# Kernel tuning notes

Measured on AMD Instinct MI355X. Metric: run time of the kernel, lower is better.

Reference implementation:

```python
import jax, jax.numpy as jnp
import numpy as np

N, D, E, P = 50000, 64, 800000, 2  # nodes, emb_dim, edges, pos dim


def setup_inputs() -> dict:
    key = jax.random.key(0)
    ks = jax.random.split(key, 20)
    s = 0.02  # gpt2-style init scale
    inp = {
        "h": jax.random.normal(ks[0], (N, D), jnp.float32),
        "pos": jax.random.uniform(ks[1], (N, P), jnp.float32),
        "h_init": jax.random.normal(ks[2], (N, D), jnp.float32),
        # edge MLP phi_e: [h_i, h_j, d2] -> D -> D
        "W_msg1": s * jax.random.normal(ks[3], (2 * D + 1, D), jnp.float32),
        "b_msg1": jnp.zeros((D,), jnp.float32),
        "W_msg2": s * jax.random.normal(ks[4], (D, D), jnp.float32),
        "b_msg2": jnp.zeros((D,), jnp.float32),
        # coord MLP phi_x: D -> D -> 1
        "W_pos1": s * jax.random.normal(ks[5], (D, D), jnp.float32),
        "b_pos1": jnp.zeros((D,), jnp.float32),
        "W_pos2": s * jax.random.normal(ks[6], (D, 1), jnp.float32),
        "b_pos2": jnp.zeros((1,), jnp.float32),
        # node MLP phi_h: [h, agg] -> D -> D
        "W_h1": s * jax.random.normal(ks[7], (2 * D, D), jnp.float32),
        "b_h1": jnp.zeros((D,), jnp.float32),
        "W_h2": s * jax.random.normal(ks[8], (D, D), jnp.float32),
        "b_h2": jnp.zeros((D,), jnp.float32),
        "edge_index": jax.random.randint(ks[9], (2, E), 0, N, jnp.int64),
    }
    return inp


def _egnn(h, pos, edge_index, W_msg1, b_msg1, W_msg2, b_msg2,
          W_pos1, b_pos1, W_pos2, b_pos2, W_h1, b_h1, W_h2, b_h2):
    src, dst = edge_index[0], edge_index[1]  # message j(src) -> i(dst)
    rel = pos[dst] - pos[src]                                  # [E,P]
    d2 = jnp.sum(rel * rel, axis=-1, keepdims=True)            # [E,1]
    m_in = jnp.concatenate([h[dst], h[src], d2], axis=-1)      # [E,2D+1]
    m = jax.nn.silu(jax.nn.silu(m_in @ W_msg1 + b_msg1) @ W_msg2 + b_msg2)  # [E,D]
    # coordinate update: mean_j rel_ij * phi_x(m_ij)
    w = jax.nn.silu(m @ W_pos1 + b_pos1) @ W_pos2 + b_pos2     # [E,1]
    n = h.shape[0]
    deg = jax.ops.segment_sum(jnp.ones((m.shape[0],), h.dtype), dst, num_segments=n)
    pos_update = jax.ops.segment_sum(rel * w, dst, num_segments=n) / jnp.maximum(deg, 1.0)[:, None]
    # feature update: phi_h([h, sum_j m_ij])
    agg = jax.ops.segment_sum(m, dst, num_segments=n)          # [N,D]
    h_update = jax.nn.silu(jnp.concatenate([h, agg], axis=-1) @ W_h1 + b_h1) @ W_h2 + b_h2
    return h_update, pos_update


def reference(h, pos, h_init, W_msg1, b_msg1, W_msg2, b_msg2,
              W_pos1, b_pos1, W_pos2, b_pos2, W_h1, b_h1, W_h2, b_h2,
              edge_index):
    # SpatialNCA.forward: add_init=True, skip_connections=True
    h = h + h_init
    h_update, pos_update = _egnn(h, pos, edge_index, W_msg1, b_msg1, W_msg2, b_msg2,
                                 W_pos1, b_pos1, W_pos2, b_pos2, W_h1, b_h1, W_h2, b_h2)
    return h + h_update, pos + pos_update
```

## Files before the change

### kernel.cpp

```cpp
#include <hip/hip_runtime.h>
#include <hip/hip_bf16.h>

#define N_NODES 50000
#define DIM 64
#define N_EDGES 800000
#define NTILES (N_EDGES / 16)
#define NODE_TILES (N_NODES / 16)

typedef short short8 __attribute__((ext_vector_type(8)));
typedef float f32x4 __attribute__((ext_vector_type(4)));

__device__ __forceinline__ float silu_f(float x) {
    return x * __builtin_amdgcn_rcpf(1.0f + __expf(-x));
}
__device__ __forceinline__ short f2bf(float f) {
    unsigned u = __builtin_bit_cast(unsigned, f);
    u += 0x7FFFu + ((u >> 16) & 1u);
    return (short)(u >> 16);
}
__device__ __forceinline__ void atom_pk_bf16(void* addr, unsigned data) {
    asm volatile("global_atomic_pk_add_bf16 %0, %1, off"
                 :: "v"((unsigned long long)(uintptr_t)addr), "v"(data) : "memory");
}

__global__ void k_init(const float* __restrict__ h, const float* __restrict__ h_init,
                       short* __restrict__ hpb, int* __restrict__ aggz,
                       float* __restrict__ posw3,
                       const void* __restrict__ eidx, int* __restrict__ eidx32) {
    __shared__ int sIs64;
    if (threadIdx.x == 0) {
        const int* e = (const int*)eidx;
        int f = 1;
        for (int k = 0; k < 64; ++k) if (e[2 * k + 1] != 0) { f = 0; break; }
        sIs64 = f;
    }
    __syncthreads();
    const int is64 = sIs64;

    int i = blockIdx.x * blockDim.x + threadIdx.x;
    int stride = gridDim.x * blockDim.x;
    for (int idx = i; idx < N_NODES * DIM; idx += stride)
        hpb[idx] = f2bf(h[idx] + h_init[idx]);
    for (int idx = i; idx < N_NODES * 32; idx += stride) aggz[idx] = 0;
    for (int idx = i; idx < N_NODES * 4; idx += stride) posw3[idx] = 0.0f;

    const long long* e64 = (const long long*)eidx;
    const int* e32 = (const int*)eidx;
    for (int idx = i; idx < 2 * N_EDGES; idx += stride)
        eidx32[idx] = is64 ? (int)e64[idx] : e32[idx];
}

__global__ __launch_bounds__(512, 6)
void k_edge(const short* __restrict__ hpb, const float* __restrict__ pos,
            const int* __restrict__ ei,
            const float* __restrict__ Wm1, const float* __restrict__ bm1,
            const float* __restrict__ Wm2, const float* __restrict__ bm2,
            const float* __restrict__ Wp1, const float* __restrict__ bp1,
            const float* __restrict__ Wp2, const float* __restrict__ bp2,
            short* __restrict__ aggb, float* __restrict__ posw3)
{
    __shared__ short sW1[8192];
    __shared__ short sW2[4096];
    __shared__ short sWp[4096];
    __shared__ short sT[8][1024];

    for (int i = threadIdx.x; i < 8192; i += 512) {
        int j = i & 7, lane = (i >> 3) & 63, nt = (i >> 9) & 3, kk = i >> 11;
        int k = kk * 32 + ((lane >> 4) << 3) + j;
        int n = (nt << 4) + (lane & 15);
        sW1[i] = f2bf(Wm1[k * 64 + n]);
    }
    for (int i = threadIdx.x; i < 4096; i += 512) {
        int j = i & 7, lane = (i >> 3) & 63, nt = (i >> 9) & 3, kk = i >> 11;
        int k = kk * 32 + ((lane >> 4) << 3) + j;
        int n = (nt << 4) + (lane & 15);
        sW2[i] = f2bf(Wm2[k * 64 + n]);
        sWp[i] = f2bf(Wp1[k * 64 + n]);
    }
    __syncthreads();

    const int lane = threadIdx.x & 63;
    const int wv   = threadIdx.x >> 6;
    const int g    = lane >> 4;
    const int c    = lane & 15;
    short* tile = &sT[wv][0];

    float bi1[4], bi2[4], bip[4], wp2r[4], w128f[4];
    #pragma unroll
    for (int nt = 0; nt < 4; ++nt) {
        bi1[nt]   = bm1[nt * 16 + c];
        bi2[nt]   = bm2[nt * 16 + c];
        bip[nt]   = bp1[nt * 16 + c];
        wp2r[nt]  = Wp2[nt * 16 + c];
        w128f[nt] = Wm1[128 * 64 + nt * 16 + c];
    }
    const float bp2v = bp2[0];

    const int gw = blockIdx.x * 8 + wv;
    const int nw = gridDim.x * 8;

    int s0 = 0, d0 = 0, s1 = 0, d1 = 0;
    float2 pd0 = {0.f, 0.f}, ps0 = {0.f, 0.f};
    short8 f0, f1, f2, f3;
    if (gw < NTILES) {
        int e = gw * 16 + c;
        s0 = ei[e]; d0 = ei[N_EDGES + e];
        pd0 = *(const float2*)(pos + (size_t)d0 * 2);
        ps0 = *(const float2*)(pos + (size_t)s0 * 2);
        f0 = *(const short8*)&hpb[(size_t)d0 * 64 + g * 8];
        f1 = *(const short8*)&hpb[(size_t)d0 * 64 + 32 + g * 8];
        f2 = *(const short8*)&hpb[(size_t)s0 * 64 + g * 8];
        f3 = *(const short8*)&hpb[(size_t)s0 * 64 + 32 + g * 8];
    }
    if (gw + nw < NTILES) {
        int e = (gw + nw) * 16 + c;
        s1 = ei[e]; d1 = ei[N_EDGES + e];
    }

    for (int t = gw; t < NTILES; t += nw) {
        const bool hasN  = (t + nw) < NTILES;
        const bool hasNN = (t + 2 * nw) < NTILES;

        float relx = pd0.x - ps0.x, rely = pd0.y - ps0.y;
        float dist2 = relx * relx + rely * rely;

        f32x4 acc[4];
        #pragma unroll
        for (int nt = 0; nt < 4; ++nt) acc[nt] = f32x4{0.f, 0.f, 0.f, 0.f};
        #pragma unroll
        for (int nt = 0; nt < 4; ++nt) {
            short8 b0 = *(const short8*)&sW1[((0 * 4 + nt) << 9) + (lane << 3)];
            short8 b1 = *(const short8*)&sW1[((1 * 4 + nt) << 9) + (lane << 3)];
            short8 b2 = *(const short8*)&sW1[((2 * 4 + nt) << 9) + (lane << 3)];
            short8 b3 = *(const short8*)&sW1[((3 * 4 + nt) << 9) + (lane << 3)];
            acc[nt] = __builtin_amdgcn_mfma_f32_16x16x32_bf16(f0, b0, acc[nt], 0, 0, 0);
            acc[nt] = __builtin_amdgcn_mfma_f32_16x16x32_bf16(f1, b1, acc[nt], 0, 0, 0);
            acc[nt] = __builtin_amdgcn_mfma_f32_16x16x32_bf16(f2, b2, acc[nt], 0, 0, 0);
            acc[nt] = __builtin_amdgcn_mfma_f32_16x16x32_bf16(f3, b3, acc[nt], 0, 0, 0);
        }

        short8 g0, g1, g2, g3;
        float2 pd1, ps1;
        if (hasN) {
            pd1 = *(const float2*)(pos + (size_t)d1 * 2);
            ps1 = *(const float2*)(pos + (size_t)s1 * 2);
            g0 = *(const short8*)&hpb[(size_t)d1 * 64 + g * 8];
            g1 = *(const short8*)&hpb[(size_t)d1 * 64 + 32 + g * 8];
            g2 = *(const short8*)&hpb[(size_t)s1 * 64 + g * 8];
            g3 = *(const short8*)&hpb[(size_t)s1 * 64 + 32 + g * 8];
        }
        int s2 = 0, d2i = 0;
        if (hasNN) {
            int e = (t + 2 * nw) * 16 + c;
            s2 = ei[e]; d2i = ei[N_EDGES + e];
        }

        float d2q[4];
        #pragma unroll
        for (int r = 0; r < 4; ++r) d2q[r] = __shfl(dist2, g * 4 + r, 64);
        #pragma unroll
        for (int nt = 0; nt < 4; ++nt) {
            #pragma unroll
            for (int r = 0; r < 4; ++r) {
                float v = silu_f(fmaf(d2q[r], w128f[nt], acc[nt][r] + bi1[nt]));
                int row = g * 4 + r;
                int idx = ((row << 6) + (nt << 4) + c) ^ ((row & 7) << 3);
                tile[idx] = f2bf(v);
            }
        }
        asm volatile("s_waitcnt lgkmcnt(0)" ::: "memory");
        __builtin_amdgcn_sched_barrier(0);

        short8 a20, a21;
        {
            int row = c;
            int b0 = ((row << 6) + (g << 3)) ^ ((row & 7) << 3);
            int b1 = ((row << 6) + 32 + (g << 3)) ^ ((row & 7) << 3);
            a20 = *(const short8*)&tile[b0];
            a21 = *(const short8*)&tile[b1];
        }
        f32x4 acc2[4];
        #pragma unroll
        for (int nt = 0; nt < 4; ++nt) acc2[nt] = f32x4{0.f, 0.f, 0.f, 0.f};
        #pragma unroll
        for (int nt = 0; nt < 4; ++nt) {
            short8 b0 = *(const short8*)&sW2[(nt << 9) + (lane << 3)];
            short8 b1 = *(const short8*)&sW2[((4 + nt) << 9) + (lane << 3)];
            acc2[nt] = __builtin_amdgcn_mfma_f32_16x16x32_bf16(a20, b0, acc2[nt], 0, 0, 0);
            acc2[nt] = __builtin_amdgcn_mfma_f32_16x16x32_bf16(a21, b1, acc2[nt], 0, 0, 0);
        }
        float mv[4][4];
        #pragma unroll
        for (int nt = 0; nt < 4; ++nt) {
            #pragma unroll
            for (int r = 0; r < 4; ++r) mv[nt][r] = silu_f(acc2[nt][r] + bi2[nt]);
        }

        asm volatile("s_waitcnt lgkmcnt(0)" ::: "memory");
        __builtin_amdgcn_sched_barrier(0);
        #pragma unroll
        for (int nt = 0; nt < 4; ++nt) {
            #pragma unroll
            for (int r = 0; r < 4; ++r) {
                int row = g * 4 + r;
                int idx = ((row << 6) + (nt << 4) + c) ^ ((row & 7) << 3);
                tile[idx] = f2bf(mv[nt][r]);
            }
        }
        #pragma unroll
        for (int r = 0; r < 4; ++r) {
            int q = g * 4 + r;
            int dstr = __shfl(d0, q, 64);
            unsigned lo = (unsigned)(unsigned short)f2bf(mv[0][r])
                        | ((unsigned)(unsigned short)f2bf(mv[1][r]) << 16);
            unsigned hi = (unsigned)(unsigned short)f2bf(mv[2][r])
                        | ((unsigned)(unsigned short)f2bf(mv[3][r]) << 16);
            char* base = (char*)aggb + (size_t)dstr * 128 + c * 4;
            atom_pk_bf16(base, lo);
            atom_pk_bf16(base + 64, hi);
        }
        asm volatile("s_waitcnt lgkmcnt(0)" ::: "memory");
        __builtin_amdgcn_sched_barrier(0);

        short8 ap0, ap1;
        {
            int row = c;
            int b0 = ((row << 6) + (g << 3)) ^ ((row & 7) << 3);
            int b1 = ((row << 6) + 32 + (g << 3)) ^ ((row & 7) << 3);
            ap0 = *(const short8*)&tile[b0];
            ap1 = *(const short8*)&tile[b1];
        }
        f32x4 acc3[4];
        #pragma unroll
        for (int nt = 0; nt < 4; ++nt) acc3[nt] = f32x4{0.f, 0.f, 0.f, 0.f};
        #pragma unroll
        for (int nt = 0; nt < 4; ++nt) {
            short8 b0 = *(const short8*)&sWp[(nt << 9) + (lane << 3)];
            short8 b1 = *(const short8*)&sWp[((4 + nt) << 9) + (lane << 3)];
            acc3[nt] = __builtin_amdgcn_mfma_f32_16x16x32_bf16(ap0, b0, acc3[nt], 0, 0, 0);
            acc3[nt] = __builtin_amdgcn_mfma_f32_16x16x32_bf16(ap1, b1, acc3[nt], 0, 0, 0);
        }
        #pragma unroll
        for (int r = 0; r < 4; ++r) {
            float part = 0.f;
            #pragma unroll
            for (int nt = 0; nt < 4; ++nt)
                part = fmaf(silu_f(acc3[nt][r] + bip[nt]), wp2r[nt], part);
            part += __shfl_xor(part, 1, 64);
            part += __shfl_xor(part, 2, 64);
            part += __shfl_xor(part, 4, 64);
            part += __shfl_xor(part, 8, 64);
            float w = part + bp2v;
            int q = g * 4 + r;
            int dstr = __shfl(d0, q, 64);
            float rx = __shfl(relx, q, 64);
            float ry = __shfl(rely, q, 64);
            if (c < 3) {
                float val = (c == 0) ? rx * w : (c == 1) ? ry * w : 1.0f;
                atomicAdd(posw3 + (size_t)dstr * 4 + c, val);
            }
        }

        s0 = s1; d0 = d1; pd0 = pd1; ps0 = ps1;
        f0 = g0; f1 = g1; f2 = g2; f3 = g3;
        s1 = s2; d1 = d2i;
    }
}

__global__ __launch_bounds__(512)
void k_node(const float* __restrict__ h, const float* __restrict__ h_init,
            const short* __restrict__ hpb, const float* __restrict__ pos,
            const short* __restrict__ aggb, const float* __restrict__ posw3,
            const float* __restrict__ Wh1, const float* __restrict__ bh1,
            const float* __restrict__ Wh2, const float* __restrict__ bh2,
            float* __restrict__ out)
{
    __shared__ short sW1[8192];
    __shared__ short sW2[4096];
    __shared__ short sT[8][1024];

    for (int i = threadIdx.x; i < 8192; i += 512) {
        int j = i & 7, lane = (i >> 3) & 63, nt = (i >> 9) & 3, kk = i >> 11;
        int ks = kk * 32 + ((lane >> 4) << 3) + j;
        int k;
        if (ks < 64) k = ks;
        else {
            int s = ks - 64;
            k = 64 + 16 * ((s & 1) + 2 * (s >> 5)) + ((s >> 1) & 15);
        }
        int n = (nt << 4) + (lane & 15);
        sW1[i] = f2bf(Wh1[k * 64 + n]);
    }
    for (int i = threadIdx.x; i < 4096; i += 512) {
        int j = i & 7, lane = (i >> 3) & 63, nt = (i >> 9) & 3, kk = i >> 11;
        int k = kk * 32 + ((lane >> 4) << 3) + j;
        int n = (nt << 4) + (lane & 15);
        sW2[i] = f2bf(Wh2[k * 64 + n]);
    }
    __syncthreads();

    const int lane = threadIdx.x & 63;
    const int wv   = threadIdx.x >> 6;
    const int g    = lane >> 4;
    const int c    = lane & 15;
    short* tile = &sT[wv][0];

    const int tl = blockIdx.x * 8 + wv;
    if (tl >= NODE_TILES) return;
    const int tb = tl * 16;

    float bi1[4], bi2[4];
    #pragma unroll
    for (int nt = 0; nt < 4; ++nt) {
        bi1[nt] = bh1[nt * 16 + c];
        bi2[nt] = bh2[nt * 16 + c];
    }

    const int node = tb + c;
    short8 a0 = *(const short8*)&hpb[(size_t)node * 64 + g * 8];
    short8 a1 = *(const short8*)&hpb[(size_t)node * 64 + 32 + g * 8];
    short8 a2 = *(const short8*)&aggb[(size_t)node * 64 + g * 8];
    short8 a3 = *(const short8*)&aggb[(size_t)node * 64 + 32 + g * 8];

    f32x4 acc[4];
    #pragma unroll
    for (int nt = 0; nt < 4; ++nt) acc[nt] = f32x4{0.f, 0.f, 0.f, 0.f};
    #pragma unroll
    for (int nt = 0; nt < 4; ++nt) {
        short8 b0 = *(const short8*)&sW1[((0 * 4 + nt) << 9) + (lane << 3)];
        short8 b1 = *(const short8*)&sW1[((1 * 4 + nt) << 9) + (lane << 3)];
        short8 b2 = *(const short8*)&sW1[((2 * 4 + nt) << 9) + (lane << 3)];
        short8 b3 = *(const short8*)&sW1[((3 * 4 + nt) << 9) + (lane << 3)];
        acc[nt] = __builtin_amdgcn_mfma_f32_16x16x32_bf16(a0, b0, acc[nt], 0, 0, 0);
        acc[nt] = __builtin_amdgcn_mfma_f32_16x16x32_bf16(a1, b1, acc[nt], 0, 0, 0);
        acc[nt] = __builtin_amdgcn_mfma_f32_16x16x32_bf16(a2, b2, acc[nt], 0, 0, 0);
        acc[nt] = __builtin_amdgcn_mfma_f32_16x16x32_bf16(a3, b3, acc[nt], 0, 0, 0);
    }
    #pragma unroll
    for (int nt = 0; nt < 4; ++nt) {
        #pragma unroll
        for (int r = 0; r < 4; ++r) {
            float v = silu_f(acc[nt][r] + bi1[nt]);
            int row = g * 4 + r;
            int idx = ((row << 6) + (nt << 4) + c) ^ ((row & 7) << 3);
            tile[idx] = f2bf(v);
        }
    }
    asm volatile("s_waitcnt lgkmcnt(0)" ::: "memory");
    __builtin_amdgcn_sched_barrier(0);

    short8 a20, a21;
    {
        int row = c;
        int b0 = ((row << 6) + (g << 3)) ^ ((row & 7) << 3);
        int b1 = ((row << 6) + 32 + (g << 3)) ^ ((row & 7) << 3);
        a20 = *(const short8*)&tile[b0];
        a21 = *(const short8*)&tile[b1];
    }
    f32x4 acc2[4];
    #pragma unroll
    for (int nt = 0; nt < 4; ++nt) acc2[nt] = f32x4{0.f, 0.f, 0.f, 0.f};
    #pragma unroll
    for (int nt = 0; nt < 4; ++nt) {
        short8 b0 = *(const short8*)&sW2[(nt << 9) + (lane << 3)];
        short8 b1 = *(const short8*)&sW2[((4 + nt) << 9) + (lane << 3)];
        acc2[nt] = __builtin_amdgcn_mfma_f32_16x16x32_bf16(a20, b0, acc2[nt], 0, 0, 0);
        acc2[nt] = __builtin_amdgcn_mfma_f32_16x16x32_bf16(a21, b1, acc2[nt], 0, 0, 0);
    }
    #pragma unroll
    for (int r = 0; r < 4; ++r) {
        int q = g * 4 + r;
        #pragma unroll
        for (int nt = 0; nt < 4; ++nt) {
            size_t idx = (size_t)(tb + q) * 64 + nt * 16 + c;
            out[idx] = h[idx] + h_init[idx] + acc2[nt][r] + bi2[nt];
        }
    }
    if (lane < 16) {
        int n2 = tb + lane;
        float dg = fmaxf(posw3[(size_t)n2 * 4 + 2], 1.0f);
        float inv = __builtin_amdgcn_rcpf(dg);
        float2 po = *(const float2*)(pos + (size_t)n2 * 2);
        float2 pw = *(const float2*)(posw3 + (size_t)n2 * 4);
        float2 res;
        res.x = po.x + pw.x * inv;
        res.y = po.y + pw.y * inv;
        *(float2*)(out + (size_t)N_NODES * DIM + (size_t)n2 * 2) = res;
    }
}

extern "C" void kernel_launch(void* const* d_in, const int* in_sizes, int n_in,
                              void* d_out, int out_size, void* d_ws, size_t ws_size,
                              hipStream_t stream) {
    const float* h      = (const float*)d_in[0];
    const float* pos    = (const float*)d_in[1];
    const float* h_init = (const float*)d_in[2];
    const float* Wm1    = (const float*)d_in[3];
    const float* bm1    = (const float*)d_in[4];
    const float* Wm2    = (const float*)d_in[5];
    const float* bm2    = (const float*)d_in[6];
    const float* Wp1    = (const float*)d_in[7];
    const float* bp1    = (const float*)d_in[8];
    const float* Wp2    = (const float*)d_in[9];
    const float* bp2    = (const float*)d_in[10];
    const float* Wh1    = (const float*)d_in[11];
    const float* bh1    = (const float*)d_in[12];
    const float* Wh2    = (const float*)d_in[13];
    const float* bh2    = (const float*)d_in[14];
    const void*  eidx   = (const void*)d_in[15];
    float* out = (float*)d_out;

    short* aggb   = (short*)d_ws;
    float* posw3  = (float*)(aggb + (size_t)N_NODES * DIM);
    short* hpb    = (short*)(posw3 + (size_t)N_NODES * 4);
    int*   eidx32 = (int*)(hpb + (size_t)N_NODES * DIM);

    k_init<<<2048, 256, 0, stream>>>(h, h_init, hpb, (int*)aggb, posw3, eidx, eidx32);
    k_edge<<<768, 512, 0, stream>>>(hpb, pos, eidx32, Wm1, bm1, Wm2, bm2,
                                    Wp1, bp1, Wp2, bp2, aggb, posw3);
    k_node<<<(NODE_TILES + 7) / 8, 512, 0, stream>>>(h, h_init, hpb, pos, aggb, posw3,
                                                     Wh1, bh1, Wh2, bh2, out);
}
```

Baseline: 222.7 us.

## Bin edges by destination before edge kernel and give blocks contiguous tile ranges

Adds a histogram, prefix-scan and scatter pass that buckets edges by destination node (bins of 32 nodes), writing packed (src,dst) pairs. The edge kernel then processes a contiguous chunk of sorted tiles per block instead of a grid-strided interleave. The intent is better locality for destination gathers and the bf16 atomic scatter into the aggregation buffer, and fewer atomic collisions spread across memory. In exchange it adds three extra launches, global atomics on 2048 counters (heavily contended), and a single-block scan.

```diff
diff --git a/kernel.cpp b/kernel.cpp
--- a/kernel.cpp
+++ b/kernel.cpp
@@ -6,6 +6,8 @@
 #define N_EDGES 800000
 #define NTILES (N_EDGES / 16)
 #define NODE_TILES (N_NODES / 16)
+#define NB 2048
+#define BIN_SHIFT 5
 
 typedef short short8 __attribute__((ext_vector_type(8)));
 typedef float f32x4 __attribute__((ext_vector_type(4)));
@@ -22,37 +24,79 @@
     asm volatile("global_atomic_pk_add_bf16 %0, %1, off"
                  :: "v"((unsigned long long)(uintptr_t)addr), "v"(data) : "memory");
 }
+__device__ __forceinline__ int probe_is64(const void* eidx) {
+    const int* e = (const int*)eidx;
+    int f = 1;
+    for (int k = 0; k < 64; ++k) if (e[2 * k + 1] != 0) { f = 0; break; }
+    return f;
+}
 
 __global__ void k_init(const float* __restrict__ h, const float* __restrict__ h_init,
                        short* __restrict__ hpb, int* __restrict__ aggz,
-                       float* __restrict__ posw3,
-                       const void* __restrict__ eidx, int* __restrict__ eidx32) {
-    __shared__ int sIs64;
-    if (threadIdx.x == 0) {
-        const int* e = (const int*)eidx;
-        int f = 1;
-        for (int k = 0; k < 64; ++k) if (e[2 * k + 1] != 0) { f = 0; break; }
-        sIs64 = f;
-    }
-    __syncthreads();
-    const int is64 = sIs64;
-
+                       float* __restrict__ posw3, int* __restrict__ hist) {
     int i = blockIdx.x * blockDim.x + threadIdx.x;
     int stride = gridDim.x * blockDim.x;
     for (int idx = i; idx < N_NODES * DIM; idx += stride)
         hpb[idx] = f2bf(h[idx] + h_init[idx]);
     for (int idx = i; idx < N_NODES * 32; idx += stride) aggz[idx] = 0;
     for (int idx = i; idx < N_NODES * 4; idx += stride) posw3[idx] = 0.0f;
-
+    for (int idx = i; idx < NB; idx += stride) hist[idx] = 0;
+}
+
+__global__ void k_hist(const void* __restrict__ eidx, int* __restrict__ hist) {
+    __shared__ int sIs64;
+    if (threadIdx.x == 0) sIs64 = probe_is64(eidx);
+    __syncthreads();
+    const int is64 = sIs64;
     const long long* e64 = (const long long*)eidx;
     const int* e32 = (const int*)eidx;
-    for (int idx = i; idx < 2 * N_EDGES; idx += stride)
-        eidx32[idx] = is64 ? (int)e64[idx] : e32[idx];
+    int i = blockIdx.x * blockDim.x + threadIdx.x;
+    int stride = gridDim.x * blockDim.x;
+    for (int e = i; e < N_EDGES; e += stride) {
+        int dst = is64 ? (int)e64[N_EDGES + e] : e32[N_EDGES + e];
+        atomicAdd(&hist[dst >> BIN_SHIFT], 1);
+    }
+}
+
+__global__ void k_prefix(const int* __restrict__ hist, int* __restrict__ cursor) {
+    __shared__ int part[1024];
+    int tid = threadIdx.x;
+    int a = hist[2 * tid], b = hist[2 * tid + 1];
+    part[tid] = a + b;
+    __syncthreads();
+    for (int off = 1; off < 1024; off <<= 1) {
+        int u = (tid >= off) ? part[tid - off] : 0;
+        __syncthreads();
+        part[tid] += u;
+        __syncthreads();
+    }
+    int excl = (tid > 0) ? part[tid - 1] : 0;
+    cursor[2 * tid]     = excl;
+    cursor[2 * tid + 1] = excl + a;
+}
+
+__global__ void k_scatter(const void* __restrict__ eidx, int* __restrict__ cursor,
+                          int2* __restrict__ sorted) {
+    __shared__ int sIs64;
+    if (threadIdx.x == 0) sIs64 = probe_is64(eidx);
+    __syncthreads();
+    const int is64 = sIs64;
+    const long long* e64 = (const long long*)eidx;
+    const int* e32 = (const int*)eidx;
+    int i = blockIdx.x * blockDim.x + threadIdx.x;
+    int stride = gridDim.x * blockDim.x;
+    for (int e = i; e < N_EDGES; e += stride) {
+        int src, dst;
+        if (is64) { src = (int)e64[e]; dst = (int)e64[N_EDGES + e]; }
+        else      { src = e32[e];      dst = e32[N_EDGES + e]; }
+        int p = atomicAdd(&cursor[dst >> BIN_SHIFT], 1);
+        sorted[p] = make_int2(src, dst);
+    }
 }
 
 __global__ __launch_bounds__(512, 6)
 void k_edge(const short* __restrict__ hpb, const float* __restrict__ pos,
-            const int* __restrict__ ei,
+            const int2* __restrict__ sorted,
             const float* __restrict__ Wm1, const float* __restrict__ bm1,
             const float* __restrict__ Wm2, const float* __restrict__ bm2,
             const float* __restrict__ Wp1, const float* __restrict__ bp1,
@@ -96,15 +140,16 @@
     }
     const float bp2v = bp2[0];
 
-    const int gw = blockIdx.x * 8 + wv;
-    const int nw = gridDim.x * 8;
+    const int tpb  = (NTILES + gridDim.x - 1) / gridDim.x;
+    const int tbeg = blockIdx.x * tpb + wv;
+    const int tend = min(blockIdx.x * tpb + tpb, NTILES);
 
     int s0 = 0, d0 = 0, s1 = 0, d1 = 0;
     float2 pd0 = {0.f, 0.f}, ps0 = {0.f, 0.f};
     short8 f0, f1, f2, f3;
-    if (gw < NTILES) {
-        int e = gw * 16 + c;
-        s0 = ei[e]; d0 = ei[N_EDGES + e];
+    if (tbeg < tend) {
+        int2 sd = sorted[tbeg * 16 + c];
+        s0 = sd.x; d0 = sd.y;
         pd0 = *(const float2*)(pos + (size_t)d0 * 2);
         ps0 = *(const float2*)(pos + (size_t)s0 * 2);
         f0 = *(const short8*)&hpb[(size_t)d0 * 64 + g * 8];
@@ -112,14 +157,14 @@
         f2 = *(const short8*)&hpb[(size_t)s0 * 64 + g * 8];
         f3 = *(const short8*)&hpb[(size_t)s0 * 64 + 32 + g * 8];
     }
-    if (gw + nw < NTILES) {
-        int e = (gw + nw) * 16 + c;
-        s1 = ei[e]; d1 = ei[N_EDGES + e];
-    }
-
-    for (int t = gw; t < NTILES; t += nw) {
-        const bool hasN  = (t + nw) < NTILES;
-        const bool hasNN = (t + 2 * nw) < NTILES;
+    if (tbeg + 8 < tend) {
+        int2 sd = sorted[(tbeg + 8) * 16 + c];
+        s1 = sd.x; d1 = sd.y;
+    }
+
+    for (int t = tbeg; t < tend; t += 8) {
+        const bool hasN  = (t + 8) < tend;
+        const bool hasNN = (t + 16) < tend;
 
         float relx = pd0.x - ps0.x, rely = pd0.y - ps0.y;
         float dist2 = relx * relx + rely * rely;
@@ -151,8 +196,8 @@
         }
         int s2 = 0, d2i = 0;
         if (hasNN) {
-            int e = (t + 2 * nw) * 16 + c;
-            s2 = ei[e]; d2i = ei[N_EDGES + e];
+            int2 sd = sorted[(t + 16) * 16 + c];
+            s2 = sd.x; d2i = sd.y;
         }
 
         float d2q[4];
@@ -413,10 +458,15 @@
     short* aggb   = (short*)d_ws;
     float* posw3  = (float*)(aggb + (size_t)N_NODES * DIM);
     short* hpb    = (short*)(posw3 + (size_t)N_NODES * 4);
-    int*   eidx32 = (int*)(hpb + (size_t)N_NODES * DIM);
-
-    k_init<<<2048, 256, 0, stream>>>(h, h_init, hpb, (int*)aggb, posw3, eidx, eidx32);
-    k_edge<<<768, 512, 0, stream>>>(hpb, pos, eidx32, Wm1, bm1, Wm2, bm2,
+    int2*  sorted = (int2*)(hpb + (size_t)N_NODES * DIM);
+    int*   hist   = (int*)(sorted + (size_t)N_EDGES);
+    int*   cursor = hist + NB;
+
+    k_init<<<2048, 256, 0, stream>>>(h, h_init, hpb, (int*)aggb, posw3, hist);
+    k_hist<<<512, 256, 0, stream>>>(eidx, hist);
+    k_prefix<<<1, 1024, 0, stream>>>(hist, cursor);
+    k_scatter<<<512, 256, 0, stream>>>(eidx, cursor, sorted);
+    k_edge<<<768, 512, 0, stream>>>(hpb, pos, sorted, Wm1, bm1, Wm2, bm2,
                                     Wp1, bp1, Wp2, bp2, aggb, posw3);
     k_node<<<(NODE_TILES + 7) / 8, 512, 0, stream>>>(h, h_init, hpb, pos, aggb, posw3,
                                                      Wh1, bh1, Wh2, bh2, out);
```

Result: slower. 455.2 us (+104.4%).
